# Performance work log

Measured on AMD Instinct MI355X. Metric: run time of the kernel, lower is better.

## Reference

```python
import jax, jax.numpy as jnp
import numpy as np

G, S, L, F, D = 128, 2048, 256, 512, 512  # groups, sample_num, max_len, n_factor, attn dim


def setup_inputs() -> dict:
    key = jax.random.key(0)
    ks = jax.random.split(key, 16)
    s1, s2, s3, s4 = 1.0 / np.sqrt(D), 1.0 / np.sqrt(256), 1.0 / np.sqrt(128), 1.0 / np.sqrt(64)
    return {
        "raw": jax.random.normal(ks[0], (G, S, L), jnp.float32),        # padded input_1, item i -> raw[i,:,:n_i]
        "info": jax.random.normal(ks[1], (G, L, F), jnp.float32),       # padded input_2
        "Wq": jax.random.normal(ks[2], (F, D), jnp.float32) * 0.05,
        "Wk": jax.random.normal(ks[3], (F, D), jnp.float32) * 0.05,
        "Wv": jax.random.normal(ks[4], (F, D), jnp.float32) * 0.05,
        "W1": jax.random.normal(ks[5], (D, 256), jnp.float32) * s1,
        "b1": jax.random.normal(ks[6], (256,), jnp.float32) * s1,
        "W2": jax.random.normal(ks[7], (256, 128), jnp.float32) * s2,
        "b2": jax.random.normal(ks[8], (128,), jnp.float32) * s2,
        "W3": jax.random.normal(ks[9], (128, 64), jnp.float32) * s3,
        "b3": jax.random.normal(ks[10], (64,), jnp.float32) * s3,
        "W4": jax.random.normal(ks[11], (64, 1), jnp.float32) * s4,
        "b4": jax.random.normal(ks[12], (1,), jnp.float32) * s4,
        "lengths": jax.random.randint(ks[13], (G,), 1, L + 1),          # ragged lengths n_i in [1, L]
        "sample_num": S,
    }


def reference(raw, info, Wq, Wk, Wv, W1, b1, W2, b2, W3, b3, W4, b4, lengths, sample_num):
    Lmax = info.shape[1]
    key_mask = jnp.arange(Lmax)[None, :] < lengths[:, None]            # [G, L] valid positions
    # per-item self-attention (batched over items, masked over padding)
    Q = jnp.einsum('glf,fd->gld', info, Wq)
    K = jnp.einsum('glf,fd->gld', info, Wk)
    V = jnp.einsum('glf,fd->gld', info, Wv)
    scores = jnp.einsum('gld,gmd->glm', Q, K)
    scores = jnp.where(key_mask[:, None, :], scores, -jnp.inf)
    attn = jax.nn.softmax(scores, axis=-1)
    ctx = jnp.einsum('glm,gmd->gld', attn, V)                          # [G, L, D]
    # 4-layer linear scorer (no nonlinearity in the original)
    h = ctx @ W1 + b1
    h = h @ W2 + b2
    h = h @ W3 + b3
    w = (h @ W4 + b4)[..., 0]                                          # [G, L]
    # original: items with n_i == 1 get score_weight = ones(1,1)
    onehot0 = (jnp.arange(Lmax) == 0).astype(w.dtype)
    w = jnp.where((lengths == 1)[:, None], onehot0[None, :], w)
    w = w * key_mask.astype(w.dtype)                                   # zero padded positions
    # per-item raw @ weight, concatenated along dim 1 -> [sample_num, G]
    out = jnp.einsum('gsl,gl->sg', raw, w)
    return out
```

## Files before the change

### kernel.cpp

```cpp
#include <hip/hip_runtime.h>
#include <hip/hip_bf16.h>
#include <cstdint>
#include <cmath>

#define GG 128
#define SS 2048
#define LL 256
#define FF 512
#define DD 512

typedef __bf16 bf16_t;
typedef __bf16 bf16x8 __attribute__((ext_vector_type(8)));
typedef __bf16 bf16x4 __attribute__((ext_vector_type(4)));
typedef float  f32x4  __attribute__((ext_vector_type(4)));

#define MiB (1024UL * 1024UL)
#define OFF_INFO_HI (0 * MiB)
#define OFF_INFO_LO (32 * MiB)
#define OFF_T_HI    (64 * MiB)
#define OFF_T_LO    (96 * MiB)
#define OFF_S       (128 * MiB)
#define OFF_WQ_HI   (160 * MiB)
#define OFF_WQ_LO   (160 * MiB + 512 * 1024)
#define OFF_WK_HI   (161 * MiB)
#define OFF_WK_LO   (161 * MiB + 512 * 1024)
#define OFF_GT_HI   (162 * MiB)
#define OFF_GT_LO   (162 * MiB + 512 * 1024)
#define OFF_VEFF    (163 * MiB)
#define OFF_VW      (164 * MiB)
#define OFF_CC      (164 * MiB + 4096)
#define OFF_U       (164 * MiB + 8192)
#define OFF_V34     (164 * MiB + 12288)
#define OFF_T2      (164 * MiB + 12800)
#define OFF_V234    (164 * MiB + 13312)
#define OFF_T3      (164 * MiB + 14336)
#define OFF_WVEC    (165 * MiB)

__device__ __forceinline__ void gload16(const bf16_t* g, bf16_t* lds) {
  __builtin_amdgcn_global_load_lds(
      (const __attribute__((address_space(1))) void*)g,
      (__attribute__((address_space(3))) void*)lds, 16, 0, 0);
}

__global__ __launch_bounds__(256) void prep_qk_kernel(
    const float* __restrict__ Wq, const float* __restrict__ Wk,
    bf16_t* __restrict__ Wq_hi, bf16_t* __restrict__ Wq_lo,
    bf16_t* __restrict__ Wk_hi, bf16_t* __restrict__ Wk_lo) {
  const int b = blockIdx.x, t = threadIdx.x;
  const float* src = (b < 256) ? Wq : Wk;
  bf16_t* dhi = (b < 256) ? Wq_hi : Wk_hi;
  bf16_t* dlo = (b < 256) ? Wq_lo : Wk_lo;
  int i = (b & 255) * 256 + t;
  float4 v = *(const float4*)&src[(size_t)i * 4];
  float x[4] = {v.x, v.y, v.z, v.w};
  bf16x4 h, l;
#pragma unroll
  for (int e = 0; e < 4; ++e) {
    h[e] = (bf16_t)x[e];
    l[e] = (bf16_t)(x[e] - (float)h[e]);
  }
  *(bf16x4*)&dhi[(size_t)i * 4] = h;
  *(bf16x4*)&dlo[(size_t)i * 4] = l;
}

__global__ __launch_bounds__(256) void fold2_kernel(
    const float* __restrict__ M0, const float* __restrict__ v0,
    float* __restrict__ out0, int N0, int K0,
    const float* __restrict__ M1, const float* __restrict__ v1,
    const float* __restrict__ bias1, float* __restrict__ out1, int N1, int K1) {
  __shared__ float red[256];
  const int t = threadIdx.x;
  const int b = blockIdx.x;
  float acc = 0.f;
  if (b < N0) {
    const float* row = M0 + (size_t)b * K0;
    for (int k = t; k < K0; k += 256) acc += row[k] * v0[k];
  } else {
    const int c = b - N0;
    for (int i = t; i < K1; i += 256) acc += v1[i] * M1[(size_t)i * N1 + c];
  }
  red[t] = acc;
  __syncthreads();
  if (t < 128) red[t] += red[t + 128];
  __syncthreads();
  if (t < 64) {
    float a = red[t] + red[t + 64];
#pragma unroll
    for (int off = 32; off > 0; off >>= 1) a += __shfl_down(a, off);
    if (t == 0) {
      if (b < N0) out0[b] = a;
      else out1[b - N0] = bias1[b - N0] + a;
    }
  }
}

__global__ __launch_bounds__(256) void cast_veff_kernel(
    const float* __restrict__ info, const float* __restrict__ vweff,
    const int* __restrict__ lengths, bf16_t* __restrict__ hi,
    bf16_t* __restrict__ lo, float* __restrict__ veff) {
  __shared__ float vw[512];
  const int t = threadIdx.x, lane = t & 63, wv = t >> 6;
  vw[t] = vweff[t];
  vw[256 + t] = vweff[256 + t];
  __syncthreads();
  const int row = blockIdx.x * 4 + wv;
  const float* ip = info + (size_t)row * 512 + lane * 8;
  const float4 a = *(const float4*)ip;
  const float4 b = *(const float4*)(ip + 4);
  float x[8] = {a.x, a.y, a.z, a.w, b.x, b.y, b.z, b.w};
  bf16x8 h, l;
#pragma unroll
  for (int e = 0; e < 8; ++e) {
    h[e] = (bf16_t)x[e];
    l[e] = (bf16_t)(x[e] - (float)h[e]);
  }
  *(bf16x8*)&hi[(size_t)row * 512 + lane * 8] = h;
  *(bf16x8*)&lo[(size_t)row * 512 + lane * 8] = l;
  const int d0 = lane * 8;
  float acc = 0.f;
#pragma unroll
  for (int e = 0; e < 8; ++e) acc += x[e] * vw[d0 + e];
#pragma unroll
  for (int off = 32; off > 0; off >>= 1) acc += __shfl_down(acc, off);
  const int n = lengths[row >> 8];
  if (lane == 0) veff[row] = ((row & 255) < n) ? acc : 0.f;
}

template <int BN, bool ASPLIT, bool BSPLIT, int OUTMODE, int SKIP, bool SWIZ>
__global__ __launch_bounds__(256) void gemm_bt(
    const bf16_t* __restrict__ Ahi, const bf16_t* __restrict__ Alo, int lda, long sA,
    const bf16_t* __restrict__ Bhi, const bf16_t* __restrict__ Blo, int ldb, long sB,
    void* __restrict__ C0, void* __restrict__ C1, int ldc, long sC,
    int K, const int* __restrict__ lengths) {
  constexpr int BM = 128;
  constexpr int BK = 64;
  constexpr int WM = 4;
  constexpr int WN = BN / 32;
  constexpr int PA = BM * BK;
  constexpr int PB = BN * BK;
  constexpr int ITA = BM * 8 / 256;
  constexpr int ITB = BN * 8 / 256;
  __shared__ bf16_t As[(ASPLIT ? 2 : 1) * PA];
  __shared__ bf16_t Bs[(BSPLIT ? 2 : 1) * PB];

  const int gx = gridDim.x, gy = gridDim.y;
  int wgid = blockIdx.x + gx * (blockIdx.y + gy * blockIdx.z);
  if (SWIZ) {
    const int nwg = gx * gy * (int)gridDim.z;
    const int q = nwg >> 3;
    wgid = (wgid & 7) * q + (wgid >> 3);
  }
  const int xx = wgid % gx;
  const int rem = wgid / gx;
  const int yy = rem % gy;
  const int b = rem / gy;
  const int m0 = yy * BM;
  const int n0 = xx * BN;

  if (SKIP == 1) { if ((m0 & 255) >= lengths[m0 >> 8]) return; }
  if (SKIP == 3) { int n = lengths[b]; if (m0 >= n || n0 >= n) return; }

  const int t = threadIdx.x;
  const int lane = t & 63;
  const int wave = t >> 6;
  const int wm = (wave >> 1) * 64;
  const int wn = (wave & 1) * (BN / 2);

  const bf16_t* Ah = Ahi + (size_t)b * sA;
  const bf16_t* Al = ASPLIT ? Alo + (size_t)b * sA : nullptr;
  const bf16_t* Bh = Bhi + (size_t)b * sB;
  const bf16_t* Bl = BSPLIT ? Blo + (size_t)b * sB : nullptr;

  f32x4 acc[WM][WN];
#pragma unroll
  for (int i = 0; i < WM; ++i)
#pragma unroll
    for (int j = 0; j < WN; ++j) acc[i][j] = {0.f, 0.f, 0.f, 0.f};

  const int fr = lane & 15;
  const int fs = lane >> 4;
  const int sr = t >> 3, ssl = t & 7;

  for (int k0 = 0; k0 < K; k0 += BK) {
#pragma unroll
    for (int it = 0; it < ITA; ++it) {
      const int r = sr + it * 32;
      const size_t ga = (size_t)(m0 + r) * lda + k0 + ((ssl ^ (r & 7)) << 3);
      bf16_t* dst = &As[(it * 256 + wave * 64) * 8];
      gload16(&Ah[ga], dst);
      if (ASPLIT) gload16(&Al[ga], dst + PA);
    }
#pragma unroll
    for (int it = 0; it < ITB; ++it) {
      const int r = sr + it * 32;
      const size_t ga = (size_t)(n0 + r) * ldb + k0 + ((ssl ^ (r & 7)) << 3);
      bf16_t* dst = &Bs[(it * 256 + wave * 64) * 8];
      gload16(&Bh[ga], dst);
      if (BSPLIT) gload16(&Bl[ga], dst + PB);
    }
    asm volatile("s_waitcnt vmcnt(0)" ::: "memory");
    __builtin_amdgcn_sched_barrier(0);
    __syncthreads();
#pragma unroll
    for (int kk = 0; kk < 2; ++kk) {
      bf16x8 ah[WM], al[WM], bh[WN], bl[WN];
#pragma unroll
      for (int i = 0; i < WM; ++i) {
        int r = wm + i * 16 + fr;
        int la = r * BK + (((kk * 4 + fs) ^ (r & 7)) * 8);
        ah[i] = *(const bf16x8*)&As[la];
        if (ASPLIT) al[i] = *(const bf16x8*)&As[PA + la];
      }
#pragma unroll
      for (int j = 0; j < WN; ++j) {
        int r = wn + j * 16 + fr;
        int la = r * BK + (((kk * 4 + fs) ^ (r & 7)) * 8);
        bh[j] = *(const bf16x8*)&Bs[la];
        if (BSPLIT) bl[j] = *(const bf16x8*)&Bs[PB + la];
      }
#pragma unroll
      for (int i = 0; i < WM; ++i)
#pragma unroll
        for (int j = 0; j < WN; ++j) {
          acc[i][j] = __builtin_amdgcn_mfma_f32_16x16x32_bf16(ah[i], bh[j], acc[i][j], 0, 0, 0);
          if (BSPLIT)
            acc[i][j] = __builtin_amdgcn_mfma_f32_16x16x32_bf16(ah[i], bl[j], acc[i][j], 0, 0, 0);
          if (ASPLIT)
            acc[i][j] = __builtin_amdgcn_mfma_f32_16x16x32_bf16(al[i], bh[j], acc[i][j], 0, 0, 0);
        }
    }
    __syncthreads();
  }

#pragma unroll
  for (int i = 0; i < WM; ++i) {
#pragma unroll
    for (int j = 0; j < WN; ++j) {
      const int col = n0 + wn + j * 16 + fr;
#pragma unroll
      for (int jj = 0; jj < 4; ++jj) {
        const int row = m0 + wm + i * 16 + fs * 4 + jj;
        const float v = acc[i][j][jj];
        const size_t off = (size_t)b * sC + (size_t)row * ldc + col;
        if (OUTMODE == 0) {
          ((float*)C0)[off] = v;
        } else {
          bf16_t h = (bf16_t)v;
          ((bf16_t*)C0)[off] = h;
          ((bf16_t*)C1)[off] = (bf16_t)(v - (float)h);
        }
      }
    }
  }
}

__global__ __launch_bounds__(256) void softmax_dot_kernel(
    const float* __restrict__ S, const float* __restrict__ veff,
    const float* __restrict__ cc, const int* __restrict__ lengths,
    float* __restrict__ w) {
  const int t = threadIdx.x, lane = t & 63, wave = t >> 6;
  const int row = blockIdx.x * 4 + wave;
  const int g = row >> 8, l = row & 255;
  const int n = lengths[g];
  if (n == 1 || l >= n) {
    if (lane == 0) w[row] = (n == 1 && l == 0) ? 1.f : 0.f;
    return;
  }
  const float* srow = S + (size_t)row * 256;
  const int c0i = lane * 4;
  float4 v = *(const float4*)&srow[c0i];
  float4 vf = *(const float4*)&veff[g * 256 + c0i];
  float s[4] = {v.x, v.y, v.z, v.w};
  float ve[4] = {vf.x, vf.y, vf.z, vf.w};
  float m = -INFINITY;
#pragma unroll
  for (int e = 0; e < 4; ++e)
    if (c0i + e < n) m = fmaxf(m, s[e]);
#pragma unroll
  for (int off = 32; off > 0; off >>= 1) m = fmaxf(m, __shfl_xor(m, off));
  float sum = 0.f, dot = 0.f;
#pragma unroll
  for (int e = 0; e < 4; ++e) {
    if (c0i + e < n) {
      float ee = __expf(s[e] - m);
      sum += ee;
      dot += ee * ve[e];
    }
  }
#pragma unroll
  for (int off = 32; off > 0; off >>= 1) {
    sum += __shfl_xor(sum, off);
    dot += __shfl_xor(dot, off);
  }
  if (lane == 0) w[row] = dot / sum + cc[0];
}

__global__ __launch_bounds__(256) void out_kernel(
    const float* __restrict__ raw, const float* __restrict__ w,
    const int* __restrict__ lengths, float* __restrict__ out) {
  __shared__ float wl[LL];
  const int g = blockIdx.x;
  const int t = threadIdx.x;
  wl[t] = w[g * LL + t];
  __syncthreads();
  const int n = lengths[g];
  const int wave = t >> 6, lane = t & 63;
  const int s = blockIdx.y * 4 + wave;
  float acc = 0.f;
  if (lane * 4 < n) {
    const float4 r4 = *(const float4*)(raw + ((size_t)g * SS + s) * LL + lane * 4);
    const float4 w4v = *(const float4*)&wl[lane * 4];
    acc = r4.x * w4v.x + r4.y * w4v.y + r4.z * w4v.z + r4.w * w4v.w;
  }
#pragma unroll
  for (int off = 32; off > 0; off >>= 1) acc += __shfl_down(acc, off);
  if (lane == 0) out[(size_t)s * GG + g] = acc;
}

extern "C" void kernel_launch(void* const* d_in, const int* in_sizes, int n_in,
                              void* d_out, int out_size, void* d_ws, size_t ws_size,
                              hipStream_t stream) {
  const float* raw  = (const float*)d_in[0];
  const float* info = (const float*)d_in[1];
  const float* Wq   = (const float*)d_in[2];
  const float* Wk   = (const float*)d_in[3];
  const float* Wv   = (const float*)d_in[4];
  const float* W1   = (const float*)d_in[5];
  const float* b1   = (const float*)d_in[6];
  const float* W2   = (const float*)d_in[7];
  const float* b2   = (const float*)d_in[8];
  const float* W3   = (const float*)d_in[9];
  const float* b3   = (const float*)d_in[10];
  const float* W4   = (const float*)d_in[11];
  const float* b4   = (const float*)d_in[12];
  const int* lengths = (const int*)d_in[13];
  float* out = (float*)d_out;

  char* ws = (char*)d_ws;
  bf16_t* info_hi = (bf16_t*)(ws + OFF_INFO_HI);
  bf16_t* info_lo = (bf16_t*)(ws + OFF_INFO_LO);
  bf16_t* T_hi = (bf16_t*)(ws + OFF_T_HI);
  bf16_t* T_lo = (bf16_t*)(ws + OFF_T_LO);
  bf16_t* Wq_hi = (bf16_t*)(ws + OFF_WQ_HI);
  bf16_t* Wq_lo = (bf16_t*)(ws + OFF_WQ_LO);
  bf16_t* Wk_hi = (bf16_t*)(ws + OFF_WK_HI);
  bf16_t* Wk_lo = (bf16_t*)(ws + OFF_WK_LO);
  bf16_t* Gt_hi = (bf16_t*)(ws + OFF_GT_HI);
  bf16_t* Gt_lo = (bf16_t*)(ws + OFF_GT_LO);
  float*  S     = (float*)(ws + OFF_S);
  float*  veff  = (float*)(ws + OFF_VEFF);
  float*  vweff = (float*)(ws + OFF_VW);
  float*  cc    = (float*)(ws + OFF_CC);
  float*  u_g   = (float*)(ws + OFF_U);
  float*  v34   = (float*)(ws + OFF_V34);
  float*  t2g   = (float*)(ws + OFF_T2);
  float*  v234  = (float*)(ws + OFF_V234);
  float*  t3g   = (float*)(ws + OFF_T3);
  float*  w     = (float*)(ws + OFF_WVEC);

  dim3 blk(256);
  const int M = GG * LL;

  prep_qk_kernel<<<dim3(512), blk, 0, stream>>>(Wq, Wk, Wq_hi, Wq_lo, Wk_hi, Wk_lo);

  fold2_kernel<<<dim3(256), blk, 0, stream>>>(
      W3, W4, v34, 128, 64, W2, b1, b2, t2g, 128, 256);
  fold2_kernel<<<dim3(320), blk, 0, stream>>>(
      W2, v34, v234, 256, 128, W3, t2g, b3, t3g, 64, 128);
  fold2_kernel<<<dim3(513), blk, 0, stream>>>(
      W1, v234, u_g, 512, 256, W4, t3g, b4, cc, 1, 64);
  fold2_kernel<<<dim3(512), blk, 0, stream>>>(
      Wv, u_g, vweff, 512, 512, W4, t3g, b4, cc, 0, 64);

  cast_veff_kernel<<<dim3(M / 4), blk, 0, stream>>>(info, vweff, lengths,
                                                    info_hi, info_lo, veff);

  gemm_bt<128, true, true, 2, 0, false><<<dim3(4, 4, 1), blk, 0, stream>>>(
      Wk_hi, Wk_lo, 512, 0, Wq_hi, Wq_lo, 512, 0, Gt_hi, Gt_lo, 512, 0, 512, nullptr);

  gemm_bt<128, true, true, 2, 1, true><<<dim3(4, M / 128, 1), blk, 0, stream>>>(
      info_hi, info_lo, 512, 0, Gt_hi, Gt_lo, 512, 0, T_hi, T_lo, 512, 0, 512, lengths);

  gemm_bt<128, true, true, 0, 3, true><<<dim3(2, 2, GG), blk, 0, stream>>>(
      T_hi, T_lo, 512, 256L * 512, info_hi, info_lo, 512, 256L * 512,
      S, nullptr, 256, 256L * 256, 512, lengths);

  softmax_dot_kernel<<<dim3(M / 4), blk, 0, stream>>>(S, veff, cc, lengths, w);

  out_kernel<<<dim3(GG, SS / 4), blk, 0, stream>>>(raw, w, lengths, out);
}
```

Before: 205.2 us.

## Fuse score GEMM with masked softmax-dot into one kernel

Replaces the per-group score GEMM (which wrote an fp32 S matrix) and the separate softmax-dot kernel with one 512-thread kernel. Each block computes a 128x256 row tile of scores in registers via split-bf16 MFMA, then does the masked row max, exp-sum and veff dot product through cross-wave LDS reductions and writes w directly. This removes the S write and read round trip and one launch. In exchange the blocks are larger and there is less parallelism (256 blocks), and the kernel has no double buffering, so loads are not overlapped with compute.

```diff
diff --git a/kernel.cpp b/kernel.cpp
--- a/kernel.cpp
+++ b/kernel.cpp
@@ -19,22 +19,21 @@
 #define OFF_INFO_LO (32 * MiB)
 #define OFF_T_HI    (64 * MiB)
 #define OFF_T_LO    (96 * MiB)
-#define OFF_S       (128 * MiB)
-#define OFF_WQ_HI   (160 * MiB)
-#define OFF_WQ_LO   (160 * MiB + 512 * 1024)
-#define OFF_WK_HI   (161 * MiB)
-#define OFF_WK_LO   (161 * MiB + 512 * 1024)
-#define OFF_GT_HI   (162 * MiB)
-#define OFF_GT_LO   (162 * MiB + 512 * 1024)
-#define OFF_VEFF    (163 * MiB)
-#define OFF_VW      (164 * MiB)
-#define OFF_CC      (164 * MiB + 4096)
-#define OFF_U       (164 * MiB + 8192)
-#define OFF_V34     (164 * MiB + 12288)
-#define OFF_T2      (164 * MiB + 12800)
-#define OFF_V234    (164 * MiB + 13312)
-#define OFF_T3      (164 * MiB + 14336)
-#define OFF_WVEC    (165 * MiB)
+#define OFF_WQ_HI   (128 * MiB)
+#define OFF_WQ_LO   (128 * MiB + 512 * 1024)
+#define OFF_WK_HI   (129 * MiB)
+#define OFF_WK_LO   (129 * MiB + 512 * 1024)
+#define OFF_GT_HI   (130 * MiB)
+#define OFF_GT_LO   (130 * MiB + 512 * 1024)
+#define OFF_VEFF    (131 * MiB)
+#define OFF_VW      (132 * MiB)
+#define OFF_CC      (132 * MiB + 4096)
+#define OFF_U       (132 * MiB + 8192)
+#define OFF_V34     (132 * MiB + 12288)
+#define OFF_T2      (132 * MiB + 12800)
+#define OFF_V234    (132 * MiB + 13312)
+#define OFF_T3      (132 * MiB + 14336)
+#define OFF_WVEC    (133 * MiB)
 
 __device__ __forceinline__ void gload16(const bf16_t* g, bf16_t* lds) {
   __builtin_amdgcn_global_load_lds(
@@ -158,7 +157,6 @@
   const int n0 = xx * BN;
 
   if (SKIP == 1) { if ((m0 & 255) >= lengths[m0 >> 8]) return; }
-  if (SKIP == 3) { int n = lengths[b]; if (m0 >= n || n0 >= n) return; }
 
   const int t = threadIdx.x;
   const int lane = t & 63;
@@ -242,57 +240,163 @@
         const int row = m0 + wm + i * 16 + fs * 4 + jj;
         const float v = acc[i][j][jj];
         const size_t off = (size_t)b * sC + (size_t)row * ldc + col;
-        if (OUTMODE == 0) {
-          ((float*)C0)[off] = v;
-        } else {
-          bf16_t h = (bf16_t)v;
-          ((bf16_t*)C0)[off] = h;
-          ((bf16_t*)C1)[off] = (bf16_t)(v - (float)h);
+        bf16_t h = (bf16_t)v;
+        ((bf16_t*)C0)[off] = h;
+        ((bf16_t*)C1)[off] = (bf16_t)(v - (float)h);
+      }
+    }
+  }
+}
+
+__global__ __launch_bounds__(512) void s_softmax_kernel(
+    const bf16_t* __restrict__ Thi, const bf16_t* __restrict__ Tlo,
+    const bf16_t* __restrict__ Ihi, const bf16_t* __restrict__ Ilo,
+    const float* __restrict__ veff, const float* __restrict__ cc,
+    const int* __restrict__ lengths, float* __restrict__ w) {
+  constexpr int BM = 128, BN = 256, BK = 64;
+  constexpr int PA = BM * BK, PB = BN * BK;
+  const int g = blockIdx.y;
+  const int m0t = blockIdx.x * BM;
+  const int n = lengths[g];
+  const int t = threadIdx.x;
+  if (m0t >= n) {
+    if (t < BM) w[g * 256 + m0t + t] = 0.f;
+    return;
+  }
+  __shared__ bf16_t As[2 * PA];
+  __shared__ bf16_t Bs[2 * PB];
+  __shared__ float redmax[BM][4];
+  __shared__ float redsum[BM][4];
+  __shared__ float reddot[BM][4];
+
+  const int lane = t & 63;
+  const int wave = t >> 6;
+  const int wm = (wave >> 2) * 64;
+  const int wn = (wave & 3) * 64;
+
+  const bf16_t* Ah = Thi + ((size_t)g * 256 + m0t) * 512;
+  const bf16_t* Al = Tlo + ((size_t)g * 256 + m0t) * 512;
+  const bf16_t* Bh = Ihi + ((size_t)g * 256) * 512;
+  const bf16_t* Bl = Ilo + ((size_t)g * 256) * 512;
+
+  f32x4 acc[4][4];
+#pragma unroll
+  for (int i = 0; i < 4; ++i)
+#pragma unroll
+    for (int j = 0; j < 4; ++j) acc[i][j] = {0.f, 0.f, 0.f, 0.f};
+
+  const int fr = lane & 15;
+  const int fs = lane >> 4;
+  const int sr = t >> 3, ssl = t & 7;
+
+  for (int k0 = 0; k0 < 512; k0 += BK) {
+#pragma unroll
+    for (int it = 0; it < 2; ++it) {
+      const int r = sr + it * 64;
+      const size_t ga = (size_t)r * 512 + k0 + ((ssl ^ (r & 7)) << 3);
+      bf16_t* dst = &As[(it * 512 + wave * 64) * 8];
+      gload16(&Ah[ga], dst);
+      gload16(&Al[ga], dst + PA);
+    }
+#pragma unroll
+    for (int it = 0; it < 4; ++it) {
+      const int r = sr + it * 64;
+      const size_t ga = (size_t)r * 512 + k0 + ((ssl ^ (r & 7)) << 3);
+      bf16_t* dst = &Bs[(it * 512 + wave * 64) * 8];
+      gload16(&Bh[ga], dst);
+      gload16(&Bl[ga], dst + PB);
+    }
+    asm volatile("s_waitcnt vmcnt(0)" ::: "memory");
+    __builtin_amdgcn_sched_barrier(0);
+    __syncthreads();
+#pragma unroll
+    for (int kk = 0; kk < 2; ++kk) {
+      bf16x8 ah[4], al[4], bh[4], bl[4];
+#pragma unroll
+      for (int i = 0; i < 4; ++i) {
+        int r = wm + i * 16 + fr;
+        int la = r * BK + (((kk * 4 + fs) ^ (r & 7)) * 8);
+        ah[i] = *(const bf16x8*)&As[la];
+        al[i] = *(const bf16x8*)&As[PA + la];
+      }
+#pragma unroll
+      for (int j = 0; j < 4; ++j) {
+        int r = wn + j * 16 + fr;
+        int la = r * BK + (((kk * 4 + fs) ^ (r & 7)) * 8);
+        bh[j] = *(const bf16x8*)&Bs[la];
+        bl[j] = *(const bf16x8*)&Bs[PB + la];
+      }
+#pragma unroll
+      for (int i = 0; i < 4; ++i)
+#pragma unroll
+        for (int j = 0; j < 4; ++j) {
+          acc[i][j] = __builtin_amdgcn_mfma_f32_16x16x32_bf16(ah[i], bh[j], acc[i][j], 0, 0, 0);
+          acc[i][j] = __builtin_amdgcn_mfma_f32_16x16x32_bf16(ah[i], bl[j], acc[i][j], 0, 0, 0);
+          acc[i][j] = __builtin_amdgcn_mfma_f32_16x16x32_bf16(al[i], bh[j], acc[i][j], 0, 0, 0);
         }
-      }
-    }
-  }
-}
-
-__global__ __launch_bounds__(256) void softmax_dot_kernel(
-    const float* __restrict__ S, const float* __restrict__ veff,
-    const float* __restrict__ cc, const int* __restrict__ lengths,
-    float* __restrict__ w) {
-  const int t = threadIdx.x, lane = t & 63, wave = t >> 6;
-  const int row = blockIdx.x * 4 + wave;
-  const int g = row >> 8, l = row & 255;
-  const int n = lengths[g];
-  if (n == 1 || l >= n) {
-    if (lane == 0) w[row] = (n == 1 && l == 0) ? 1.f : 0.f;
-    return;
-  }
-  const float* srow = S + (size_t)row * 256;
-  const int c0i = lane * 4;
-  float4 v = *(const float4*)&srow[c0i];
-  float4 vf = *(const float4*)&veff[g * 256 + c0i];
-  float s[4] = {v.x, v.y, v.z, v.w};
-  float ve[4] = {vf.x, vf.y, vf.z, vf.w};
-  float m = -INFINITY;
-#pragma unroll
-  for (int e = 0; e < 4; ++e)
-    if (c0i + e < n) m = fmaxf(m, s[e]);
-#pragma unroll
-  for (int off = 32; off > 0; off >>= 1) m = fmaxf(m, __shfl_xor(m, off));
-  float sum = 0.f, dot = 0.f;
-#pragma unroll
-  for (int e = 0; e < 4; ++e) {
-    if (c0i + e < n) {
-      float ee = __expf(s[e] - m);
-      sum += ee;
-      dot += ee * ve[e];
-    }
-  }
-#pragma unroll
-  for (int off = 32; off > 0; off >>= 1) {
-    sum += __shfl_xor(sum, off);
-    dot += __shfl_xor(dot, off);
-  }
-  if (lane == 0) w[row] = dot / sum + cc[0];
+    }
+    __syncthreads();
+  }
+
+#pragma unroll
+  for (int i = 0; i < 4; ++i) {
+#pragma unroll
+    for (int jj = 0; jj < 4; ++jj) {
+      float m = -INFINITY;
+#pragma unroll
+      for (int j = 0; j < 4; ++j) {
+        const int c = wn + j * 16 + fr;
+        if (c < n) m = fmaxf(m, acc[i][j][jj]);
+      }
+#pragma unroll
+      for (int off = 1; off < 16; off <<= 1) m = fmaxf(m, __shfl_xor(m, off));
+      if (fr == 0) redmax[wm + i * 16 + fs * 4 + jj][wave & 3] = m;
+    }
+  }
+  __syncthreads();
+#pragma unroll
+  for (int i = 0; i < 4; ++i) {
+#pragma unroll
+    for (int jj = 0; jj < 4; ++jj) {
+      const int r = wm + i * 16 + fs * 4 + jj;
+      const float M = fmaxf(fmaxf(redmax[r][0], redmax[r][1]),
+                            fmaxf(redmax[r][2], redmax[r][3]));
+      float s = 0.f, d = 0.f;
+#pragma unroll
+      for (int j = 0; j < 4; ++j) {
+        const int c = wn + j * 16 + fr;
+        if (c < n) {
+          const float e = __expf(acc[i][j][jj] - M);
+          s += e;
+          d += e * veff[g * 256 + c];
+        }
+      }
+#pragma unroll
+      for (int off = 1; off < 16; off <<= 1) {
+        s += __shfl_xor(s, off);
+        d += __shfl_xor(d, off);
+      }
+      if (fr == 0) {
+        redsum[r][wave & 3] = s;
+        reddot[r][wave & 3] = d;
+      }
+    }
+  }
+  __syncthreads();
+  if (t < BM) {
+    const int grow = m0t + t;
+    float val;
+    if (n == 1) {
+      val = (grow == 0) ? 1.f : 0.f;
+    } else if (grow >= n) {
+      val = 0.f;
+    } else {
+      const float s = redsum[t][0] + redsum[t][1] + redsum[t][2] + redsum[t][3];
+      const float d = reddot[t][0] + reddot[t][1] + reddot[t][2] + reddot[t][3];
+      val = d / s + cc[0];
+    }
+    w[g * 256 + grow] = val;
+  }
 }
 
 __global__ __launch_bounds__(256) void out_kernel(
@@ -347,7 +451,6 @@
   bf16_t* Wk_lo = (bf16_t*)(ws + OFF_WK_LO);
   bf16_t* Gt_hi = (bf16_t*)(ws + OFF_GT_HI);
   bf16_t* Gt_lo = (bf16_t*)(ws + OFF_GT_LO);
-  float*  S     = (float*)(ws + OFF_S);
   float*  veff  = (float*)(ws + OFF_VEFF);
   float*  vweff = (float*)(ws + OFF_VW);
   float*  cc    = (float*)(ws + OFF_CC);
@@ -381,11 +484,8 @@
   gemm_bt<128, true, true, 2, 1, true><<<dim3(4, M / 128, 1), blk, 0, stream>>>(
       info_hi, info_lo, 512, 0, Gt_hi, Gt_lo, 512, 0, T_hi, T_lo, 512, 0, 512, lengths);
 
-  gemm_bt<128, true, true, 0, 3, true><<<dim3(2, 2, GG), blk, 0, stream>>>(
-      T_hi, T_lo, 512, 256L * 512, info_hi, info_lo, 512, 256L * 512,
-      S, nullptr, 256, 256L * 256, 512, lengths);
-
-  softmax_dot_kernel<<<dim3(M / 4), blk, 0, stream>>>(S, veff, cc, lengths, w);
+  s_softmax_kernel<<<dim3(2, GG), dim3(512), 0, stream>>>(
+      T_hi, T_lo, info_hi, info_lo, veff, cc, lengths, w);
 
   out_kernel<<<dim3(GG, SS / 4), blk, 0, stream>>>(raw, w, lengths, out);
 }
```

Measured after the change: 210.7 us. 2.7% more time.
